# Optimization experiments

Hardware: AMD Instinct MI355X
Metric: run time of the kernel (lower is better)

## Reference

```python
import jax, jax.numpy as jnp
import numpy as np

N = 10000   # nodes
E = 160000  # edges
F_IN = 768  # input features
EPS = 1e-5


def _norm_weights(src, dst, ew, n):
    # sym-normalized scaled Laplacian with lambda_max=2: T_hat = -D^{-1/2} A D^{-1/2}
    deg = jax.ops.segment_sum(ew, src, num_segments=n)
    deg_safe = jnp.where(deg > 0, deg, 1.0)
    dis = jnp.where(deg > 0, jax.lax.rsqrt(deg_safe), 0.0)
    return -dis[src] * ew * dis[dst]


def _cheb(x, src, dst, norm, Ws, b, n):
    # PyG ChebConv forward: out = sum_k lin_k(T_k(L_hat) x) + bias
    def prop(h):  # gather -> weight -> scatter-add
        return jax.ops.segment_sum(norm[:, None] * h[src], dst, num_segments=n)
    Tx0 = x
    out = Tx0 @ Ws[0]
    if len(Ws) > 1:
        Tx1 = prop(Tx0)
        out = out + Tx1 @ Ws[1]
        for W in Ws[2:]:
            Tx2 = 2.0 * prop(Tx1) - Tx0
            out = out + Tx2 @ W
            Tx0, Tx1 = Tx1, Tx2
    return out + b


def _bn(x, g, b):
    # training-mode batch norm over the node dim
    mu = x.mean(axis=0)
    var = x.var(axis=0)
    return (x - mu) * jax.lax.rsqrt(var + EPS) * g + b


def _glorot(k, shp):
    lim = (6.0 / (shp[0] + shp[1])) ** 0.5
    return jax.random.uniform(k, shp, jnp.float32, -lim, lim)


def setup_inputs() -> dict:
    key = jax.random.key(0)
    ks = jax.random.split(key, 12)
    inp = {
        "x": jax.random.normal(ks[0], (N, F_IN), jnp.float32),
        "edge_index": jax.random.randint(ks[1], (2, E), 0, N, jnp.int64),
        "edge_attr": jax.random.uniform(ks[2], (E,), jnp.float32),
        "W1_0": _glorot(ks[3], (F_IN, 512)), "b1": jnp.zeros((512,), jnp.float32),
        "g1": jnp.ones((512,), jnp.float32), "be1": jnp.zeros((512,), jnp.float32),
        "W2_0": _glorot(ks[4], (512, 256)), "W2_1": _glorot(ks[5], (512, 256)),
        "b2": jnp.zeros((256,), jnp.float32),
        "g2": jnp.ones((256,), jnp.float32), "be2": jnp.zeros((256,), jnp.float32),
        "W3_0": _glorot(ks[6], (256, 128)), "W3_1": _glorot(ks[7], (256, 128)),
        "W3_2": _glorot(ks[8], (256, 128)), "b3": jnp.zeros((128,), jnp.float32),
        "g3": jnp.ones((128,), jnp.float32), "be3": jnp.zeros((128,), jnp.float32),
        "fcW": _glorot(ks[9], (128, 6)), "fcb": jnp.zeros((6,), jnp.float32),
    }
    return inp


def reference(x, edge_index, edge_attr,
              W1_0, b1, g1, be1,
              W2_0, W2_1, b2, g2, be2,
              W3_0, W3_1, W3_2, b3, g3, be3,
              fcW, fcb):
    src, dst = edge_index[0], edge_index[1]
    norm = _norm_weights(src, dst, edge_attr, N)
    h = jax.nn.relu(_bn(_cheb(x, src, dst, norm, [W1_0], b1, N), g1, be1))
    h = jax.nn.relu(_bn(_cheb(h, src, dst, norm, [W2_0, W2_1], b2, N), g2, be2))
    h = _bn(_cheb(h, src, dst, norm, [W3_0, W3_1, W3_2], b3, N), g3, be3)
    return jax.nn.log_softmax(h @ fcW + fcb, axis=1)
```

## Files before the change

kernel.cpp:

```cpp
#include <hip/hip_runtime.h>
#include <hip/hip_bf16.h>
#include <cstdint>

#define N_NODES 10000
#define N_EDGES 160000
#define MPAD    10112

typedef __attribute__((ext_vector_type(8))) short short8;
typedef __attribute__((ext_vector_type(4))) float floatx4;
typedef unsigned short us;


__device__ __forceinline__ us bf16_rn(float f) {
    union { float f; unsigned u; } c{f};
    unsigned r = c.u + 0x7FFF + ((c.u >> 16) & 1);
    return (us)(r >> 16);
}
__device__ __forceinline__ float bf16_to_f(us h) {
    union { unsigned u; float f; } c{(unsigned)h << 16};
    return c.f;
}
__device__ __forceinline__ unsigned pack_hi2(float a, float b) {
    return (unsigned)bf16_rn(a) | ((unsigned)bf16_rn(b) << 16);
}
__device__ __forceinline__ unsigned pack_lo2(float a, float b) {
    float ra = a - bf16_to_f(bf16_rn(a));
    float rb = b - bf16_to_f(bf16_rn(b));
    return (unsigned)bf16_rn(ra) | ((unsigned)bf16_rn(rb) << 16);
}

__device__ __forceinline__ void gload_lds16(const void* g, void* l) {
    __builtin_amdgcn_global_load_lds(
        (const __attribute__((address_space(1))) unsigned int*)g,
        (__attribute__((address_space(3))) unsigned int*)l, 16, 0, 0);
}



__global__ void deg_kernel(const int* __restrict__ src, const int* __restrict__ dst,
                           const float* __restrict__ ew,
                           float* __restrict__ deg, int* __restrict__ cnt) {
    int e = blockIdx.x * blockDim.x + threadIdx.x;
    if (e >= N_EDGES) return;
    atomicAdd(&deg[src[e]], ew[e]);
    atomicAdd(&cnt[dst[e]], 1);
}

__global__ __launch_bounds__(1024) void dis_scan_kernel(const float* __restrict__ deg,
                                                        const int* __restrict__ cnt,
                                                        float* __restrict__ dis,
                                                        int* __restrict__ rowptr) {
    const int t = threadIdx.x;
    if (blockIdx.x != 0) {
        int n = (blockIdx.x - 1) * 1024 + t;
        if (n < N_NODES) {
            float d = deg[n];
            dis[n] = d > 0.f ? rsqrtf(d) : 0.f;
        }
        return;
    }
    __shared__ int wsum[16];
    const int lane = t & 63, wid = t >> 6;
    int carry = 0;
    for (int base = 0; base < N_NODES; base += 1024) {
        int i = base + t;
        int v = (i < N_NODES) ? cnt[i] : 0;
        int s = v;
        #pragma unroll
        for (int off = 1; off < 64; off <<= 1) {
            int u = __shfl_up(s, off);
            if (lane >= off) s += u;
        }
        if (lane == 63) wsum[wid] = s;
        __syncthreads();
        int woff = 0, tot = 0;
        for (int ww = 0; ww < 16; ++ww) {
            int xv = wsum[ww];
            if (ww < wid) woff += xv;
            tot += xv;
        }
        if (i < N_NODES) rowptr[i + 1] = carry + woff + s;
        carry += tot;
        __syncthreads();
    }
    if (t == 0) rowptr[0] = 0;
}

__global__ void fill_kernel(const int* __restrict__ src, const int* __restrict__ dst,
                            const float* __restrict__ ew, const float* __restrict__ dis,
                            const int* __restrict__ rowptr, int* __restrict__ fill,
                            int* __restrict__ csr_src, float* __restrict__ csr_w) {
    int e = blockIdx.x * blockDim.x + threadIdx.x;
    if (e >= N_EDGES) return;
    int s = src[e], d = dst[e];
    int pos = rowptr[d] + atomicAdd(&fill[d], 1);
    csr_src[pos] = s;
    csr_w[pos] = -dis[s] * ew[e] * dis[d];
}


__device__ __forceinline__ void cvt_x_body(int bx, int k16, const float* __restrict__ x,
                                           us* __restrict__ Ap) {
    int m = bx * 256 + threadIdx.x;
    if (m >= N_NODES) return;
    const float4* p = (const float4*)(x + (size_t)m * 768 + k16 * 16);
    float4 v0 = p[0], v1 = p[1], v2 = p[2], v3 = p[3];
    uint4 hi0, hi1, lo0, lo1;
    hi0.x = pack_hi2(v0.x, v0.y); hi0.y = pack_hi2(v0.z, v0.w);
    hi0.z = pack_hi2(v1.x, v1.y); hi0.w = pack_hi2(v1.z, v1.w);
    hi1.x = pack_hi2(v2.x, v2.y); hi1.y = pack_hi2(v2.z, v2.w);
    hi1.z = pack_hi2(v3.x, v3.y); hi1.w = pack_hi2(v3.z, v3.w);
    lo0.x = pack_lo2(v0.x, v0.y); lo0.y = pack_lo2(v0.z, v0.w);
    lo0.z = pack_lo2(v1.x, v1.y); lo0.w = pack_lo2(v1.z, v1.w);
    lo1.x = pack_lo2(v2.x, v2.y); lo1.y = pack_lo2(v2.z, v2.w);
    lo1.z = pack_lo2(v3.x, v3.y); lo1.w = pack_lo2(v3.z, v3.w);
    int pa = m >> 7, rr = m & 127;
    int kt = k16 >> 1, kqb = (k16 & 1) * 2;
    size_t th = ((size_t)pa * 48 + kt) * 4096;
    size_t tl = ((size_t)pa * 48 + 24 + kt) * 4096;
    *(uint4*)&Ap[th + ((kqb + 0) * 128 + rr) * 8] = hi0;
    *(uint4*)&Ap[th + ((kqb + 1) * 128 + rr) * 8] = hi1;
    *(uint4*)&Ap[tl + ((kqb + 0) * 128 + rr) * 8] = lo0;
    *(uint4*)&Ap[tl + ((kqb + 1) * 128 + rr) * 8] = lo1;
}

__device__ __forceinline__ void cvt_w_body(int bx, int k16, const float* __restrict__ W,
                                           us* __restrict__ Bp, int K, int N) {
    int n = bx * 256 + threadIdx.x;
    if (n >= N) return;
    float v[16];
    #pragma unroll
    for (int j = 0; j < 16; ++j) v[j] = W[(size_t)(k16 * 16 + j) * N + n];
    uint4 hi0, hi1, lo0, lo1;
    hi0.x = pack_hi2(v[0], v[1]);  hi0.y = pack_hi2(v[2], v[3]);
    hi0.z = pack_hi2(v[4], v[5]);  hi0.w = pack_hi2(v[6], v[7]);
    hi1.x = pack_hi2(v[8], v[9]);  hi1.y = pack_hi2(v[10], v[11]);
    hi1.z = pack_hi2(v[12], v[13]); hi1.w = pack_hi2(v[14], v[15]);
    lo0.x = pack_lo2(v[0], v[1]);  lo0.y = pack_lo2(v[2], v[3]);
    lo0.z = pack_lo2(v[4], v[5]);  lo0.w = pack_lo2(v[6], v[7]);
    lo1.x = pack_lo2(v[8], v[9]);  lo1.y = pack_lo2(v[10], v[11]);
    lo1.z = pack_lo2(v[12], v[13]); lo1.w = pack_lo2(v[14], v[15]);
    int pb = n >> 6, c = n & 63;
    int NKTB = K >> 4;
    int kt = k16 >> 1, kqb = (k16 & 1) * 2;
    size_t th = ((size_t)pb * NKTB + kt) * 2048;
    size_t tl = ((size_t)pb * NKTB + (K >> 5) + kt) * 2048;
    *(uint4*)&Bp[th + ((kqb + 0) * 64 + c) * 8] = hi0;
    *(uint4*)&Bp[th + ((kqb + 1) * 64 + c) * 8] = hi1;
    *(uint4*)&Bp[tl + ((kqb + 0) * 64 + c) * 8] = lo0;
    *(uint4*)&Bp[tl + ((kqb + 1) * 64 + c) * 8] = lo1;
}

__global__ __launch_bounds__(256) void cvt_all_kernel(const float* __restrict__ x,
                                                      us* __restrict__ A1,
                                                      const float* __restrict__ W1,
                                                      us* __restrict__ B1T,
                                                      const float* __restrict__ W2a,
                                                      const float* __restrict__ W2b,
                                                      us* __restrict__ B2T,
                                                      const float* __restrict__ W3a,
                                                      const float* __restrict__ W3b,
                                                      const float* __restrict__ W3c,
                                                      us* __restrict__ B3T) {
    int b = blockIdx.x;
    if (b < 1920) { cvt_x_body(b % 40, b / 40, x, A1); return; }
    b -= 1920;
    if (b < 96)  { cvt_w_body(b & 1, b >> 1, W1, B1T, 768, 512); return; }
    b -= 96;
    if (b < 32)  { cvt_w_body(0, b, W2a, B2T, 512, 256); return; }
    b -= 32;
    if (b < 32)  { cvt_w_body(0, b, W2b, B2T + (size_t)4 * 32 * 2048, 512, 256); return; }
    b -= 32;
    if (b < 16)  { cvt_w_body(0, b, W3a, B3T, 256, 128); return; }
    b -= 16;
    if (b < 16)  { cvt_w_body(0, b, W3b, B3T + (size_t)2 * 16 * 2048, 256, 128); return; }
    b -= 16;
    cvt_w_body(0, b, W3c, B3T + (size_t)4 * 16 * 2048, 256, 128);
}

__global__ __launch_bounds__(256) void bn_relu_cvt_kernel(const float* __restrict__ G,
                                                          const float* __restrict__ sums,
                                                          const float* __restrict__ g,
                                                          const float* __restrict__ be,
                                                          us* __restrict__ Ap, int F) {
    const int k16 = blockIdx.y;
    int m = blockIdx.x * 256 + threadIdx.x;
    if (m >= N_NODES) return;
    const float invM = 1.0f / (float)N_NODES;
    float sc[16], sh[16];
    #pragma unroll
    for (int j = 0; j < 16; ++j) {
        int c = k16 * 16 + j;
        float mu = sums[c] * invM;
        float s = g[c] * rsqrtf(sums[F + c] * invM - mu * mu + 1e-5f);
        sc[j] = s;
        sh[j] = be[c] - mu * s;
    }
    const float4* p = (const float4*)(G + (size_t)m * F + k16 * 16);
    float v[16];
    #pragma unroll
    for (int q = 0; q < 4; ++q) {
        float4 t4 = p[q];
        v[q * 4 + 0] = t4.x; v[q * 4 + 1] = t4.y;
        v[q * 4 + 2] = t4.z; v[q * 4 + 3] = t4.w;
    }
    #pragma unroll
    for (int j = 0; j < 16; ++j) v[j] = fmaxf(v[j] * sc[j] + sh[j], 0.f);
    uint4 hi0, hi1, lo0, lo1;
    hi0.x = pack_hi2(v[0], v[1]);  hi0.y = pack_hi2(v[2], v[3]);
    hi0.z = pack_hi2(v[4], v[5]);  hi0.w = pack_hi2(v[6], v[7]);
    hi1.x = pack_hi2(v[8], v[9]);  hi1.y = pack_hi2(v[10], v[11]);
    hi1.z = pack_hi2(v[12], v[13]); hi1.w = pack_hi2(v[14], v[15]);
    lo0.x = pack_lo2(v[0], v[1]);  lo0.y = pack_lo2(v[2], v[3]);
    lo0.z = pack_lo2(v[4], v[5]);  lo0.w = pack_lo2(v[6], v[7]);
    lo1.x = pack_lo2(v[8], v[9]);  lo1.y = pack_lo2(v[10], v[11]);
    lo1.z = pack_lo2(v[12], v[13]); lo1.w = pack_lo2(v[14], v[15]);
    int pa = m >> 7, rr = m & 127;
    int NKT = F >> 4;
    int kt = k16 >> 1, kqb = (k16 & 1) * 2;
    size_t th = ((size_t)pa * NKT + kt) * 4096;
    size_t tl = ((size_t)pa * NKT + (F >> 5) + kt) * 4096;
    *(uint4*)&Ap[th + ((kqb + 0) * 128 + rr) * 8] = hi0;
    *(uint4*)&Ap[th + ((kqb + 1) * 128 + rr) * 8] = hi1;
    *(uint4*)&Ap[tl + ((kqb + 0) * 128 + rr) * 8] = lo0;
    *(uint4*)&Ap[tl + ((kqb + 1) * 128 + rr) * 8] = lo1;
}


__global__ __launch_bounds__(256, 4) void mfma_gemm_kernel(
        const us* __restrict__ Ap,
        const us* __restrict__ BpT,
        float* __restrict__ C,
        int M, int Ksub, int Nc, int ncb,
        float* __restrict__ sums) {
    __shared__ us As[4096];
    __shared__ us Bs[2048];
    const int t = threadIdx.x;
    const int w = t >> 6, l = t & 63;

    int nwg = gridDim.x, bid = blockIdx.x;
    int q = nwg >> 3, r = nwg & 7;
    int xcd = bid & 7, idx = bid >> 3;
    int wgid = (xcd < r ? xcd * (q + 1) : r * (q + 1) + (xcd - r) * q) + idx;
    const int row0 = (wgid / ncb) * 128;
    const int col0 = (wgid % ncb) * 64;

    const int NKTA = Ksub >> 4;
    const int Ktot = 3 * Ksub;
    const int wr = w >> 1, wc = w & 1;
    const int lr = l & 15, kq = l >> 4;

    const size_t Abase = (size_t)(row0 >> 7) * NKTA * 4096;
    const size_t Bbase = (size_t)(col0 >> 6) * NKTA * 2048;

    floatx4 acc[4][2] = {};

    for (int k0 = 0; k0 < Ktot; k0 += 32) {
        int kA = (k0 < 2 * Ksub) ? k0 : k0 - 2 * Ksub;
        int kB = (k0 < Ksub)     ? k0 : k0 - Ksub;
        const us* At = Ap + Abase + (size_t)(kA >> 5) * 4096;
        const us* Bt = BpT + Bbase + (size_t)(kB >> 5) * 2048;
        gload_lds16(At + (w * 64 + l) * 8,       (char*)As + w * 1024);
        gload_lds16(At + ((w + 4) * 64 + l) * 8, (char*)As + (w + 4) * 1024);
        gload_lds16(Bt + (w * 64 + l) * 8,       (char*)Bs + w * 1024);
        __syncthreads();
        short8 af[4], bfr[2];
        #pragma unroll
        for (int m = 0; m < 4; ++m)
            af[m] = *(const short8*)&As[(kq * 128 + wr * 64 + m * 16 + lr) * 8];
        #pragma unroll
        for (int n = 0; n < 2; ++n)
            bfr[n] = *(const short8*)&Bs[(kq * 64 + wc * 32 + n * 16 + lr) * 8];
        #pragma unroll
        for (int m = 0; m < 4; ++m)
            #pragma unroll
            for (int n = 0; n < 2; ++n)
                acc[m][n] = __builtin_amdgcn_mfma_f32_16x16x32_bf16(
                    af[m], bfr[n], acc[m][n], 0, 0, 0);
        __syncthreads();
    }

    #pragma unroll
    for (int m = 0; m < 4; ++m) {
        int rb = row0 + wr * 64 + m * 16 + kq * 4;
        #pragma unroll
        for (int j = 0; j < 4; ++j) {
            int rr = rb + j;
            if (rr < M) {
                #pragma unroll
                for (int n = 0; n < 2; ++n)
                    C[(size_t)rr * Nc + col0 + wc * 32 + n * 16 + lr] = acc[m][n][j];
            }
        }
    }

    if (sums) {
        float s[2] = {0.f, 0.f}, qv[2] = {0.f, 0.f};
        #pragma unroll
        for (int m = 0; m < 4; ++m)
            #pragma unroll
            for (int n = 0; n < 2; ++n)
                #pragma unroll
                for (int j = 0; j < 4; ++j) {
                    float v = acc[m][n][j];
                    s[n] += v; qv[n] += v * v;
                }
        float* red = (float*)As;
        int g8 = wr * 4 + kq;
        #pragma unroll
        for (int n = 0; n < 2; ++n) {
            int c = wc * 32 + n * 16 + lr;
            red[g8 * 128 + c * 2 + 0] = s[n];
            red[g8 * 128 + c * 2 + 1] = qv[n];
        }
        __syncthreads();
        if (t < 128) {
            float tot = 0.f;
            #pragma unroll
            for (int g = 0; g < 8; ++g) tot += red[g * 128 + t];
            int c = t >> 1, e = t & 1;
            atomicAdd(&sums[e * 512 + col0 + c], tot);
        }
    }
}


__global__ __launch_bounds__(256) void prop_l2_kernel(const float* __restrict__ G2,
                                                      const int* __restrict__ rowptr,
                                                      const int* __restrict__ csr_s,
                                                      const float* __restrict__ csr_w,
                                                      float* __restrict__ out2) {
    const int g = threadIdx.x >> 6, lane = threadIdx.x & 63;
    const int n = blockIdx.x * 4 + g;
    const int f4 = lane * 4;
    float4 acc = {0.f, 0.f, 0.f, 0.f};
    int e = rowptr[n];
    const int e1 = rowptr[n + 1];
    for (; e + 1 < e1; e += 2) {
        int s0 = csr_s[e], s1 = csr_s[e + 1];
        float w0 = csr_w[e], w1 = csr_w[e + 1];
        float4 a = *(const float4*)&G2[(size_t)s0 * 512 + 256 + f4];
        float4 b = *(const float4*)&G2[(size_t)s1 * 512 + 256 + f4];
        acc.x += w0 * a.x + w1 * b.x; acc.y += w0 * a.y + w1 * b.y;
        acc.z += w0 * a.z + w1 * b.z; acc.w += w0 * a.w + w1 * b.w;
    }
    if (e < e1) {
        float w0 = csr_w[e];
        float4 a = *(const float4*)&G2[(size_t)csr_s[e] * 512 + 256 + f4];
        acc.x += w0 * a.x; acc.y += w0 * a.y; acc.z += w0 * a.z; acc.w += w0 * a.w;
    }
    float4 base = *(const float4*)&G2[(size_t)n * 512 + f4];
    acc.x += base.x; acc.y += base.y; acc.z += base.z; acc.w += base.w;
    *(float4*)&out2[(size_t)n * 256 + f4] = acc;
}

__global__ __launch_bounds__(256) void bn_stats256_kernel(const float* __restrict__ h,
                                                          float* __restrict__ sums) {
    const int t = threadIdx.x;
    int r0 = blockIdx.x * 20, r1 = min(r0 + 20, N_NODES);
    float s = 0.f, q = 0.f;
    for (int r = r0; r < r1; ++r) {
        float v = h[(size_t)r * 256 + t];
        s += v; q += v * v;
    }
    atomicAdd(&sums[t], s);
    atomicAdd(&sums[256 + t], q);
}

__global__ __launch_bounds__(256) void prop3a_kernel(const float* __restrict__ G3,
                                                     const int* __restrict__ rowptr,
                                                     const int* __restrict__ csr_s,
                                                     const float* __restrict__ csr_w,
                                                     float* __restrict__ T) {
    const int g = threadIdx.x >> 5, lane = threadIdx.x & 31;
    const int n = blockIdx.x * 8 + g;
    const int f4 = lane * 4;
    float4 acc = {0.f, 0.f, 0.f, 0.f};
    int e = rowptr[n];
    const int e1 = rowptr[n + 1];
    for (; e + 1 < e1; e += 2) {
        int s0 = csr_s[e], s1 = csr_s[e + 1];
        float w0 = csr_w[e], w1 = csr_w[e + 1];
        float4 a = *(const float4*)&G3[(size_t)s0 * 384 + 256 + f4];
        float4 b = *(const float4*)&G3[(size_t)s1 * 384 + 256 + f4];
        acc.x += w0 * a.x + w1 * b.x; acc.y += w0 * a.y + w1 * b.y;
        acc.z += w0 * a.z + w1 * b.z; acc.w += w0 * a.w + w1 * b.w;
    }
    if (e < e1) {
        float w0 = csr_w[e];
        float4 a = *(const float4*)&G3[(size_t)csr_s[e] * 384 + 256 + f4];
        acc.x += w0 * a.x; acc.y += w0 * a.y; acc.z += w0 * a.z; acc.w += w0 * a.w;
    }
    *(float4*)&T[(size_t)n * 128 + f4] = acc;
}

__global__ __launch_bounds__(256) void prop3b_combine_kernel(const float* __restrict__ G3,
                                                             const float* __restrict__ T,
                                                             const int* __restrict__ rowptr,
                                                             const int* __restrict__ csr_s,
                                                             const float* __restrict__ csr_w,
                                                             float* __restrict__ Fbuf,
                                                             float* __restrict__ sums) {
    __shared__ float red_s[8][128];
    __shared__ float red_q[8][128];
    const int g = threadIdx.x >> 5, lane = threadIdx.x & 31;
    const int n = blockIdx.x * 8 + g;
    const int f4 = lane * 4;
    float4 acc = {0.f, 0.f, 0.f, 0.f};
    int e = rowptr[n];
    const int e1 = rowptr[n + 1];
    for (; e < e1; ++e) {
        int s = csr_s[e];
        float w0 = csr_w[e];
        float4 a = *(const float4*)&G3[(size_t)s * 384 + 128 + f4];
        float4 b = *(const float4*)&T[(size_t)s * 128 + f4];
        acc.x += w0 * (a.x + 2.f * b.x); acc.y += w0 * (a.y + 2.f * b.y);
        acc.z += w0 * (a.z + 2.f * b.z); acc.w += w0 * (a.w + 2.f * b.w);
    }
    float4 p = *(const float4*)&G3[(size_t)n * 384 + f4];
    float4 r = *(const float4*)&G3[(size_t)n * 384 + 256 + f4];
    float4 v;
    v.x = p.x - r.x + acc.x; v.y = p.y - r.y + acc.y;
    v.z = p.z - r.z + acc.z; v.w = p.w - r.w + acc.w;
    *(float4*)&Fbuf[(size_t)n * 128 + f4] = v;
    red_s[g][f4 + 0] = v.x; red_s[g][f4 + 1] = v.y;
    red_s[g][f4 + 2] = v.z; red_s[g][f4 + 3] = v.w;
    red_q[g][f4 + 0] = v.x * v.x; red_q[g][f4 + 1] = v.y * v.y;
    red_q[g][f4 + 2] = v.z * v.z; red_q[g][f4 + 3] = v.w * v.w;
    __syncthreads();
    const int t = threadIdx.x;
    if (t < 128) {
        float s = 0.f, q = 0.f;
        #pragma unroll
        for (int gg = 0; gg < 8; ++gg) { s += red_s[gg][t]; q += red_q[gg][t]; }
        atomicAdd(&sums[t], s);
        atomicAdd(&sums[128 + t], q);
    }
}


__global__ __launch_bounds__(256) void final_kernel(const float* __restrict__ h,
                                                    const float* __restrict__ sums,
                                                    const float* __restrict__ g3,
                                                    const float* __restrict__ be3,
                                                    const float* __restrict__ fcW,
                                                    const float* __restrict__ fcb,
                                                    float* __restrict__ out) {
    const int t = threadIdx.x, lane = t & 63, wid = t >> 6;
    const int r = blockIdx.x * 4 + wid;
    if (r >= N_NODES) return;
    const float invM = 1.0f / (float)N_NODES;
    float v[6] = {0.f, 0.f, 0.f, 0.f, 0.f, 0.f};
    #pragma unroll
    for (int kk = 0; kk < 2; ++kk) {
        int k = lane + kk * 64;
        float mu = sums[k] * invM;
        float sc = g3[k] * rsqrtf(sums[128 + k] * invM - mu * mu + 1e-5f);
        float sh = be3[k] - mu * sc;
        float x = h[(size_t)r * 128 + k] * sc + sh;
        #pragma unroll
        for (int j = 0; j < 6; ++j) v[j] += x * fcW[k * 6 + j];
    }
    #pragma unroll
    for (int j = 0; j < 6; ++j)
        #pragma unroll
        for (int off = 32; off > 0; off >>= 1) v[j] += __shfl_down(v[j], off);
    if (lane == 0) {
        #pragma unroll
        for (int j = 0; j < 6; ++j) v[j] += fcb[j];
        float m = v[0];
        #pragma unroll
        for (int j = 1; j < 6; ++j) m = fmaxf(m, v[j]);
        float s = 0.f;
        #pragma unroll
        for (int j = 0; j < 6; ++j) s += expf(v[j] - m);
        float l = m + logf(s);
        #pragma unroll
        for (int j = 0; j < 6; ++j) out[r * 6 + j] = v[j] - l;
    }
}


extern "C" void kernel_launch(void* const* d_in, const int* in_sizes, int n_in,
                              void* d_out, int out_size, void* d_ws, size_t ws_size,
                              hipStream_t stream) {
    (void)in_sizes; (void)n_in; (void)out_size; (void)ws_size;
    const float* x   = (const float*)d_in[0];
    const int*   ei  = (const int*)d_in[1];
    const float* ea  = (const float*)d_in[2];
    const float* W1  = (const float*)d_in[3];
    const float* g1  = (const float*)d_in[5];
    const float* be1 = (const float*)d_in[6];
    const float* W2a = (const float*)d_in[7];
    const float* W2b = (const float*)d_in[8];
    const float* g2  = (const float*)d_in[10];
    const float* be2 = (const float*)d_in[11];
    const float* W3a = (const float*)d_in[12];
    const float* W3b = (const float*)d_in[13];
    const float* W3c = (const float*)d_in[14];
    const float* g3  = (const float*)d_in[16];
    const float* be3 = (const float*)d_in[17];
    const float* fcW = (const float*)d_in[18];
    const float* fcb = (const float*)d_in[19];
    float* out = (float*)d_out;

    const int* src = ei;
    const int* dst = ei + N_EDGES;

    char* w = (char*)d_ws;
    size_t off = 0;
    auto alloc = [&](size_t bytes) -> void* {
        void* p = w + off;
        off += (bytes + 4095) & ~(size_t)4095;
        return p;
    };
    float* deg    = (float*)alloc(N_NODES * 4);
    int*   cnt    = (int*)  alloc(N_NODES * 4);
    int*   fillc  = (int*)  alloc(N_NODES * 4);
    float* sums1  = (float*)alloc(1024 * 4);
    float* sums2  = (float*)alloc(1024 * 4);
    float* sums3  = (float*)alloc(1024 * 4);
    size_t zero_bytes = off;
    float* dis    = (float*)alloc(N_NODES * 4);
    int*   rowptr = (int*)  alloc((N_NODES + 1) * 4);
    int*   csr_s  = (int*)  alloc(N_EDGES * 4);
    float* csr_w  = (float*)alloc(N_EDGES * 4);
    us* B1T = (us*)alloc((size_t)512 * 1536 * 2);
    us* B2T = (us*)alloc((size_t)512 * 1024 * 2);
    us* B3T = (us*)alloc((size_t)384 * 512 * 2);
    us* slotA = (us*)alloc((size_t)MPAD * 1536 * 2);
    float* slotG = (float*)alloc((size_t)N_NODES * 512 * 4);
    float* slotC = (float*)alloc((size_t)N_NODES * 256 * 4);
    float* bufF  = (float*)alloc((size_t)N_NODES * 128 * 4);

    us* A1 = slotA;
    us* A2 = slotA;
    us* A3 = slotA;
    float* G1 = slotG;
    float* G2 = slotG;
    float* G3 = slotG;
    float* out2 = slotC;
    float* bufT = slotC;

    hipMemsetAsync(d_ws, 0, zero_bytes, stream);

    deg_kernel<<<N_EDGES / 256, 256, 0, stream>>>(src, dst, ea, deg, cnt);
    dis_scan_kernel<<<40, 1024, 0, stream>>>(deg, cnt, dis, rowptr);
    fill_kernel<<<N_EDGES / 256, 256, 0, stream>>>(src, dst, ea, dis, rowptr, fillc,
                                                   csr_s, csr_w);

    cvt_all_kernel<<<2128, 256, 0, stream>>>(x, A1, W1, B1T, W2a, W2b, B2T,
                                             W3a, W3b, W3c, B3T);

    mfma_gemm_kernel<<<632, 256, 0, stream>>>(A1, B1T, G1, N_NODES, 768, 512, 8, sums1);
    bn_relu_cvt_kernel<<<dim3(40, 32), 256, 0, stream>>>(G1, sums1, g1, be1, A2, 512);

    mfma_gemm_kernel<<<632, 256, 0, stream>>>(A2, B2T, G2, N_NODES, 512, 512, 8, nullptr);
    prop_l2_kernel<<<2500, 256, 0, stream>>>(G2, rowptr, csr_s, csr_w, out2);
    bn_stats256_kernel<<<500, 256, 0, stream>>>(out2, sums2);
    bn_relu_cvt_kernel<<<dim3(40, 16), 256, 0, stream>>>(out2, sums2, g2, be2, A3, 256);

    mfma_gemm_kernel<<<474, 256, 0, stream>>>(A3, B3T, G3, N_NODES, 256, 384, 6, nullptr);
    prop3a_kernel<<<1250, 256, 0, stream>>>(G3, rowptr, csr_s, csr_w, bufT);
    prop3b_combine_kernel<<<1250, 256, 0, stream>>>(G3, bufT, rowptr, csr_s, csr_w,
                                                    bufF, sums3);

    final_kernel<<<2500, 256, 0, stream>>>(bufF, sums3, g3, be3, fcW, fcb, out);
}
```

Measured before the change: 385.3 us.

## Double-buffer LDS in MFMA GEMM and stage two K-tiles per barrier

The GEMM kernel now keeps two LDS buffers and prefetches the next pair of 32-wide K tiles while computing on the current pair. This halves the number of barriers and overlaps global-to-LDS loads with MFMA work. LDS use per block grows from 12 KB to 48 KB and launch bounds drop to 3 blocks per SM, which may lower occupancy. The loop assumes the number of K tiles is even.

```diff
diff --git a/kernel.cpp b/kernel.cpp
--- a/kernel.cpp
+++ b/kernel.cpp
@@ -227,14 +227,14 @@
 }
 
 
-__global__ __launch_bounds__(256, 4) void mfma_gemm_kernel(
+__global__ __launch_bounds__(256, 3) void mfma_gemm_kernel(
         const us* __restrict__ Ap,
         const us* __restrict__ BpT,
         float* __restrict__ C,
         int M, int Ksub, int Nc, int ncb,
         float* __restrict__ sums) {
-    __shared__ us As[4096];
-    __shared__ us Bs[2048];
+    __shared__ us As[2][8192];
+    __shared__ us Bs[2][4096];
     const int t = threadIdx.x;
     const int w = t >> 6, l = t & 63;
 
@@ -246,38 +246,56 @@
     const int col0 = (wgid % ncb) * 64;
 
     const int NKTA = Ksub >> 4;
-    const int Ktot = 3 * Ksub;
+    const int nt = (3 * Ksub) >> 5;
     const int wr = w >> 1, wc = w & 1;
     const int lr = l & 15, kq = l >> 4;
 
-    const size_t Abase = (size_t)(row0 >> 7) * NKTA * 4096;
-    const size_t Bbase = (size_t)(col0 >> 6) * NKTA * 2048;
-
-    floatx4 acc[4][2] = {};
-
-    for (int k0 = 0; k0 < Ktot; k0 += 32) {
+    const us* Abase = Ap + (size_t)(row0 >> 7) * NKTA * 4096;
+    const us* Bbase = BpT + (size_t)(col0 >> 6) * NKTA * 2048;
+
+    auto stage = [&](int buf, int kt) {
+        int k0 = kt << 5;
         int kA = (k0 < 2 * Ksub) ? k0 : k0 - 2 * Ksub;
         int kB = (k0 < Ksub)     ? k0 : k0 - Ksub;
-        const us* At = Ap + Abase + (size_t)(kA >> 5) * 4096;
-        const us* Bt = BpT + Bbase + (size_t)(kB >> 5) * 2048;
-        gload_lds16(At + (w * 64 + l) * 8,       (char*)As + w * 1024);
-        gload_lds16(At + ((w + 4) * 64 + l) * 8, (char*)As + (w + 4) * 1024);
-        gload_lds16(Bt + (w * 64 + l) * 8,       (char*)Bs + w * 1024);
-        __syncthreads();
-        short8 af[4], bfr[2];
-        #pragma unroll
-        for (int m = 0; m < 4; ++m)
-            af[m] = *(const short8*)&As[(kq * 128 + wr * 64 + m * 16 + lr) * 8];
-        #pragma unroll
-        for (int n = 0; n < 2; ++n)
-            bfr[n] = *(const short8*)&Bs[(kq * 64 + wc * 32 + n * 16 + lr) * 8];
-        #pragma unroll
-        for (int m = 0; m < 4; ++m)
+        const us* At = Abase + (size_t)(kA >> 5) * 4096;
+        const us* Bt = Bbase + (size_t)(kB >> 5) * 2048;
+        char* adst = (char*)As[buf] + (kt & 1) * 8192;
+        char* bdst = (char*)Bs[buf] + (kt & 1) * 4096;
+        gload_lds16(At + (w * 64 + l) * 8,       adst + w * 1024);
+        gload_lds16(At + ((w + 4) * 64 + l) * 8, adst + (w + 4) * 1024);
+        gload_lds16(Bt + (w * 64 + l) * 8,       bdst + w * 1024);
+    };
+
+    floatx4 acc[4][2] = {};
+
+    stage(0, 0); stage(0, 1);
+    __syncthreads();
+    int cur = 0;
+    for (int kt2 = 0; kt2 < (nt >> 1); ++kt2) {
+        if (kt2 + 1 < (nt >> 1)) {
+            stage(cur ^ 1, kt2 * 2 + 2);
+            stage(cur ^ 1, kt2 * 2 + 3);
+        }
+        #pragma unroll
+        for (int sub = 0; sub < 2; ++sub) {
+            const us* Ac = &As[cur][sub * 4096];
+            const us* Bc = &Bs[cur][sub * 2048];
+            short8 af[4], bfr[2];
+            #pragma unroll
+            for (int m = 0; m < 4; ++m)
+                af[m] = *(const short8*)&Ac[(kq * 128 + wr * 64 + m * 16 + lr) * 8];
             #pragma unroll
             for (int n = 0; n < 2; ++n)
-                acc[m][n] = __builtin_amdgcn_mfma_f32_16x16x32_bf16(
-                    af[m], bfr[n], acc[m][n], 0, 0, 0);
+                bfr[n] = *(const short8*)&Bc[(kq * 64 + wc * 32 + n * 16 + lr) * 8];
+            #pragma unroll
+            for (int m = 0; m < 4; ++m)
+                #pragma unroll
+                for (int n = 0; n < 2; ++n)
+                    acc[m][n] = __builtin_amdgcn_mfma_f32_16x16x32_bf16(
+                        af[m], bfr[n], acc[m][n], 0, 0, 0);
+        }
         __syncthreads();
+        cur ^= 1;
     }
 
     #pragma unroll
```

Result: faster. 357.2 us (-7.3%).
